# Kernel tuning notes

Measured on AMD Instinct MI355X. Metric: run time of the kernel, lower is better.

The kernel has to match this reference:

```python
import jax, jax.numpy as jnp
import numpy as np

H = 1024          # hidden_size
A = 8             # num_actions
T = 64            # timesteps
N = 256           # batch (num envs)


def _gru_cell(x, h, Wih, Whh, bih, bhh):
    # torch.nn.GRUCell math; gate order (r, z, n)
    gi = x @ Wih.T + bih           # [N, 3H]
    gh = h @ Whh.T + bhh           # [N, 3H]
    i_r, i_z, i_n = jnp.split(gi, 3, axis=1)
    h_r, h_z, h_n = jnp.split(gh, 3, axis=1)
    r = jax.nn.sigmoid(i_r + h_r)
    z = jax.nn.sigmoid(i_z + h_z)
    n = jnp.tanh(i_n + r * h_n)
    return (1.0 - z) * n + z * h


def setup_inputs() -> dict:
    key = jax.random.key(0)
    ks = jax.random.split(key, 12)
    s = 0.02
    return {
        "c": jax.random.normal(ks[0], (T * N, H), jnp.float32),
        "hxs": jax.random.normal(ks[1], (N, 3 * H), jnp.float32),
        "masks": jnp.ones((T * N, 1), jnp.float32),
        "prev_action_one_hot": jnp.zeros((T * N, A), jnp.float32).at[jnp.arange(T * N), jax.random.randint(ks[2], (T * N,), 0, A)].set(1.0),
        "h_gru_Wih": s * jax.random.normal(ks[3], (3 * H, H), jnp.float32),
        "h_gru_Whh": s * jax.random.normal(ks[4], (3 * H, H), jnp.float32),
        "h_gru_bih": jnp.zeros((3 * H,), jnp.float32),
        "h_gru_bhh": jnp.zeros((3 * H,), jnp.float32),
        "f_gru_Wih": s * jax.random.normal(ks[5], (3 * H, H), jnp.float32),
        "f_gru_Whh": s * jax.random.normal(ks[6], (3 * H, H), jnp.float32),
        "f_gru_bih": jnp.zeros((3 * H,), jnp.float32),
        "f_gru_bhh": jnp.zeros((3 * H,), jnp.float32),
        "p_W": s * jax.random.normal(ks[7], (2 * H, 2 * H + A), jnp.float32),
        "p_b": jnp.zeros((2 * H,), jnp.float32),
        "q_W": s * jax.random.normal(ks[8], (2 * H, 2 * H + A), jnp.float32),
        "q_b": jnp.zeros((2 * H,), jnp.float32),
    }


def reference(c, hxs, masks, prev_action_one_hot,
              h_gru_Wih, h_gru_Whh, h_gru_bih, h_gru_bhh,
              f_gru_Wih, f_gru_Whh, f_gru_bih, f_gru_bhh,
              p_W, p_b, q_W, q_b):
    c3 = c.reshape(T, N, H)
    m3 = masks.reshape(T, N, 1)
    a3 = prev_action_one_hot.reshape(T, N, A)
    f0 = hxs[:, :H]
    h0 = hxs[:, H:2 * H]
    q0 = hxs[:, 2 * H:]

    def step(carry, xs):
        f, h, q_mu = carry
        c_t, m_t, a_t = xs
        p_in = jnp.concatenate([h, q_mu, a_t], axis=1) * m_t
        p_dist = p_in @ p_W.T + p_b                     # [N, 2H]
        p_mu = p_dist[:, :H]
        q_in = jnp.concatenate([f, c_t, a_t], axis=1) * m_t
        q_dist = q_in @ q_W.T + q_b                     # [N, 2H]
        q_mu_new = q_dist[:, :H]
        f_new = _gru_cell(c_t, f * m_t, f_gru_Wih, f_gru_Whh, f_gru_bih, f_gru_bhh)
        h_new = _gru_cell(p_mu, h * m_t, h_gru_Wih, h_gru_Whh, h_gru_bih, h_gru_bhh)
        return (f_new, h_new, q_mu_new), (p_dist, q_dist)

    (f, h, q_mu), (p_all, q_all) = jax.lax.scan(step, (f0, h0, q0), (c3, m3, a3))
    acc_p = p_all.reshape(T * N, 2 * H)
    acc_q = q_all.reshape(T * N, 2 * H)
    hxs_out = jnp.concatenate([f, h, q_mu], axis=1)
    return acc_p, acc_q, hxs_out
```

## Files before the change

### kernel.cpp

```cpp
#include <hip/hip_runtime.h>
#include <math.h>

typedef __attribute__((ext_vector_type(8))) __bf16 bf16x8;
typedef __attribute__((ext_vector_type(4))) float f32x4;

constexpr int H = 1024, T = 64, NB = 256, TWOH = 2048, THREEH = 3072;
constexpr long long OFF_Q  = 33554432LL;
constexpr long long OFF_HX = 67108864LL;
constexpr int LA = 6;

constexpr int R_PWH = 0, R_PWQ = 2048, R_QWF = 4096, R_QWC = 6144,
              R_FWIH = 8192, R_FWHH = 11264, R_HWIH = 14336, R_HWHH = 17408;

#define LD4(p) (*reinterpret_cast<const float4*>(p))

__device__ __forceinline__ float sigf(float x) { return 1.0f / (1.0f + expf(-x)); }

__device__ __forceinline__ void gload16(const void* g, void* l) {
    __builtin_amdgcn_global_load_lds(
        (const __attribute__((address_space(1))) uint32_t*)g,
        (__attribute__((address_space(3))) uint32_t*)l, 16, 0, 0);
}

__device__ __forceinline__ void st_bf_swz(__bf16* base, int n, int k, float v) {
    base[(size_t)n * 1024 + (((k >> 3) ^ (n & 7)) << 3) + (k & 7)] = (__bf16)v;
}

#define FRAGOFF(rloc, gl) (((rloc) << 7) + ((((gl)) ^ ((rloc) & 7)) << 4))

template<int RT>
__device__ __forceinline__ void stage_tile(const char* g, char* l, int kb, int tid) {
    #pragma unroll
    for (int i = 0; i < RT / 32; ++i) {
        const int L = i * 4096 + tid * 16;
        gload16(g + (size_t)(L >> 7) * 2048 + (size_t)kb * 128 + (L & 127), l + L);
    }
}

__device__ __forceinline__ void mm128(
    int tid, char* sA, char* sB,
    const char* A0, const char* B0, int n0,
    const char* A1, const char* B1, int n1,
    f32x4 (&acc)[2][4])
{
    const int lane = tid & 63, w = tid >> 6;
    const int l15 = lane & 15, lg = lane >> 4;
    const int wr = w >> 1, wc = w & 1;
    const int nit = n0 + n1;
    int aoff[2][2], boff[4][2];
    #pragma unroll
    for (int fr = 0; fr < 2; ++fr)
        #pragma unroll
        for (int kk = 0; kk < 2; ++kk)
            aoff[fr][kk] = FRAGOFF(wr * 32 + fr * 16 + l15, kk * 4 + lg);
    #pragma unroll
    for (int fc = 0; fc < 4; ++fc)
        #pragma unroll
        for (int kk = 0; kk < 2; ++kk)
            boff[fc][kk] = FRAGOFF(wc * 64 + fc * 16 + l15, kk * 4 + lg);

    stage_tile<64>(A0, sA, 0, tid);
    stage_tile<128>(B0, sB, 0, tid);
    for (int kb = 0; kb < nit; ++kb) {
        const int kn = kb + 1;
        if (kn < nit) {
            const char* An = (kn < n0) ? A0 : A1;
            const char* Bn = (kn < n0) ? B0 : B1;
            const int kl = (kn < n0) ? kn : kn - n0;
            stage_tile<64>(An, sA + (kn & 1) * 8192, kl, tid);
            stage_tile<128>(Bn, sB + (kn & 1) * 16384, kl, tid);
            asm volatile("s_waitcnt vmcnt(6)" ::: "memory");
        } else {
            asm volatile("s_waitcnt vmcnt(0)" ::: "memory");
        }
        __builtin_amdgcn_s_barrier();
        __builtin_amdgcn_sched_barrier(0);
        char* Ab = sA + (kb & 1) * 8192;
        char* Bb = sB + (kb & 1) * 16384;
        bf16x8 af[2][2], bv[4][2];
        #pragma unroll
        for (int fr = 0; fr < 2; ++fr)
            #pragma unroll
            for (int kk = 0; kk < 2; ++kk)
                af[fr][kk] = *reinterpret_cast<const bf16x8*>(Ab + aoff[fr][kk]);
        #pragma unroll
        for (int fc = 0; fc < 4; ++fc)
            #pragma unroll
            for (int kk = 0; kk < 2; ++kk)
                bv[fc][kk] = *reinterpret_cast<const bf16x8*>(Bb + boff[fc][kk]);
        __builtin_amdgcn_s_setprio(1);
        #pragma unroll
        for (int kk = 0; kk < 2; ++kk)
            #pragma unroll
            for (int fr = 0; fr < 2; ++fr)
                #pragma unroll
                for (int fc = 0; fc < 4; ++fc)
                    acc[fr][fc] = __builtin_amdgcn_mfma_f32_16x16x32_bf16(
                        af[fr][kk], bv[fc][kk], acc[fr][fc], 0, 0, 0);
        __builtin_amdgcn_s_setprio(0);
        __builtin_amdgcn_s_barrier();
        __builtin_amdgcn_sched_barrier(0);
    }
}

__device__ __forceinline__ void mm32g1(
    int tid, char* sA, char* sB,
    const char* A, const char* Bg,
    f32x4 (&aR)[2], f32x4 (&aZ)[2], f32x4 (&aN)[2])
{
    const int lane = tid & 63, w = tid >> 6;
    const int l15 = lane & 15, lg = lane >> 4;
    const int wr = w >> 1, wc = w & 1;
    int aoff[2], boff[2][2];
    #pragma unroll
    for (int kk = 0; kk < 2; ++kk)
        aoff[kk] = FRAGOFF(wr * 16 + l15, kk * 4 + lg);
    #pragma unroll
    for (int fc = 0; fc < 2; ++fc)
        #pragma unroll
        for (int kk = 0; kk < 2; ++kk)
            boff[fc][kk] = FRAGOFF(wc * 32 + fc * 16 + l15, kk * 4 + lg);

    auto stg = [&](int buf, int kb) {
        stage_tile<32>(A, sA + buf * 4096, kb, tid);
        #pragma unroll
        for (int g = 0; g < 3; ++g)
            stage_tile<64>(Bg + (size_t)g * 2097152, sB + buf * 24576 + g * 8192, kb, tid);
    };
    stg(0, 0);
    for (int kb = 0; kb < 16; ++kb) {
        if (kb + 1 < 16) {
            stg((kb + 1) & 1, kb + 1);
            asm volatile("s_waitcnt vmcnt(7)" ::: "memory");
        } else {
            asm volatile("s_waitcnt vmcnt(0)" ::: "memory");
        }
        __builtin_amdgcn_s_barrier();
        __builtin_amdgcn_sched_barrier(0);
        char* Ab = sA + (kb & 1) * 4096;
        char* Bb = sB + (kb & 1) * 24576;
        bf16x8 af[2];
        #pragma unroll
        for (int kk = 0; kk < 2; ++kk)
            af[kk] = *reinterpret_cast<const bf16x8*>(Ab + aoff[kk]);
        bf16x8 bvr[2][2], bvz[2][2], bvn[2][2];
        #pragma unroll
        for (int fc = 0; fc < 2; ++fc)
            #pragma unroll
            for (int kk = 0; kk < 2; ++kk) {
                bvr[fc][kk] = *reinterpret_cast<const bf16x8*>(Bb + boff[fc][kk]);
                bvz[fc][kk] = *reinterpret_cast<const bf16x8*>(Bb + 8192 + boff[fc][kk]);
                bvn[fc][kk] = *reinterpret_cast<const bf16x8*>(Bb + 16384 + boff[fc][kk]);
            }
        __builtin_amdgcn_s_setprio(1);
        #pragma unroll
        for (int kk = 0; kk < 2; ++kk)
            #pragma unroll
            for (int fc = 0; fc < 2; ++fc) {
                aR[fc] = __builtin_amdgcn_mfma_f32_16x16x32_bf16(af[kk], bvr[fc][kk], aR[fc], 0, 0, 0);
                aZ[fc] = __builtin_amdgcn_mfma_f32_16x16x32_bf16(af[kk], bvz[fc][kk], aZ[fc], 0, 0, 0);
                aN[fc] = __builtin_amdgcn_mfma_f32_16x16x32_bf16(af[kk], bvn[fc][kk], aN[fc], 0, 0, 0);
            }
        __builtin_amdgcn_s_setprio(0);
        __builtin_amdgcn_s_barrier();
        __builtin_amdgcn_sched_barrier(0);
    }
}

__device__ __forceinline__ void do_xq(int slice, int i, int tid, char* sA, char* sB,
    const char* cbfB, const char* Wb, const float* act, const float* qW, float* out)
{
    const int lane = tid & 63, w = tid >> 6;
    const int l15 = lane & 15, lg = lane >> 4;
    const int wr = w >> 1, wc = w & 1;
    const int row0 = (i >> 4) * 64, col0 = (i & 15) * 128;
    const size_t grow0 = (size_t)slice * NB + row0;
    f32x4 acc[2][4] = {};
    mm128(tid, sA, sB, cbfB + grow0 * 2048, Wb + (size_t)(R_QWC + col0) * 2048, 16,
          nullptr, nullptr, 0, acc);
    #pragma unroll
    for (int fc = 0; fc < 4; ++fc) {
        const int gc = col0 + wc * 64 + fc * 16 + l15;
        const float* wp = qW + (size_t)gc * 2056 + 2048;
        float4 x0 = LD4(wp), x1 = LD4(wp + 4);
        #pragma unroll
        for (int fr = 0; fr < 2; ++fr)
            #pragma unroll
            for (int j = 0; j < 4; ++j) {
                const size_t n = grow0 + wr * 32 + fr * 16 + lg * 4 + j;
                const float* ar = act + n * 8;
                float4 a0 = LD4(ar), a1 = LD4(ar + 4);
                float dot = a0.x * x0.x + a0.y * x0.y + a0.z * x0.z + a0.w * x0.w
                          + a1.x * x1.x + a1.y * x1.y + a1.z * x1.z + a1.w * x1.w;
                out[OFF_Q + n * TWOH + gc] = acc[fr][fc][j] + dot;
            }
    }
}

__device__ __forceinline__ void do_gf(int slice, int i, int tid, char* sA, char* sB,
    const char* cbfB, const char* Wb, __bf16* Gfb)
{
    const int lane = tid & 63, w = tid >> 6;
    const int l15 = lane & 15, lg = lane >> 4;
    const int wr = w >> 1, wc = w & 1;
    const int row0 = (i / 24) * 64, col0 = (i % 24) * 128;
    f32x4 acc[2][4] = {};
    mm128(tid, sA, sB, cbfB + ((size_t)slice * NB + row0) * 2048,
          Wb + (size_t)(R_FWIH + col0) * 2048, 16, nullptr, nullptr, 0, acc);
    __bf16* gdst = Gfb + (size_t)(slice & 7) * NB * THREEH;
    #pragma unroll
    for (int fc = 0; fc < 4; ++fc) {
        const int gc = col0 + wc * 64 + fc * 16 + l15;
        #pragma unroll
        for (int fr = 0; fr < 2; ++fr)
            #pragma unroll
            for (int j = 0; j < 4; ++j) {
                const int n = row0 + wr * 32 + fr * 16 + lg * 4 + j;
                gdst[(size_t)n * THREEH + gc] = (__bf16)acc[fr][fc][j];
            }
    }
}

__global__ __launch_bounds__(256) void wcvt_k(
    const float* __restrict__ pW, const float* __restrict__ qW,
    const float* __restrict__ fWih, const float* __restrict__ fWhh,
    const float* __restrict__ hWih, const float* __restrict__ hWhh,
    __bf16* __restrict__ Wbf)
{
    const long i = (long)blockIdx.x * 256 + threadIdx.x;
    const int row = (int)(i >> 7);
    const int G   = (int)i & 127;
    const float* src; int stride; int koff = 0; int r;
    if (row < 2048)       { src = pW;   stride = 2056; koff = 0;    r = row; }
    else if (row < 4096)  { src = pW;   stride = 2056; koff = 1024; r = row - 2048; }
    else if (row < 6144)  { src = qW;   stride = 2056; koff = 0;    r = row - 4096; }
    else if (row < 8192)  { src = qW;   stride = 2056; koff = 1024; r = row - 6144; }
    else if (row < 11264) { src = fWih; stride = 1024; r = row - 8192; }
    else if (row < 14336) { src = fWhh; stride = 1024; r = row - 11264; }
    else if (row < 17408) { src = hWih; stride = 1024; r = row - 14336; }
    else                  { src = hWhh; stride = 1024; r = row - 17408; }
    const float* p = src + (long)r * stride + koff + G * 8;
    float4 a = LD4(p), b = LD4(p + 4);
    bf16x8 v;
    v[0] = (__bf16)a.x; v[1] = (__bf16)a.y; v[2] = (__bf16)a.z; v[3] = (__bf16)a.w;
    v[4] = (__bf16)b.x; v[5] = (__bf16)b.y; v[6] = (__bf16)b.z; v[7] = (__bf16)b.w;
    *reinterpret_cast<bf16x8*>(Wbf + (size_t)row * 1024 + ((G ^ (row & 7)) << 3)) = v;
}

__global__ __launch_bounds__(256) void ccvt_k(const float* __restrict__ c,
                                              __bf16* __restrict__ cbf) {
    const long i = (long)blockIdx.x * 256 + threadIdx.x;
    const int row = (int)(i >> 7);
    const int G   = (int)i & 127;
    const float* p = c + (size_t)row * 1024 + G * 8;
    float4 a = LD4(p), b = LD4(p + 4);
    bf16x8 v;
    v[0] = (__bf16)a.x; v[1] = (__bf16)a.y; v[2] = (__bf16)a.z; v[3] = (__bf16)a.w;
    v[4] = (__bf16)b.x; v[5] = (__bf16)b.y; v[6] = (__bf16)b.z; v[7] = (__bf16)b.w;
    *reinterpret_cast<bf16x8*>(cbf + (size_t)row * 1024 + ((G ^ (row & 7)) << 3)) = v;
}

__global__ __launch_bounds__(256) void init2_k(
    const float* __restrict__ hxs, const float* __restrict__ masks,
    float* __restrict__ fst0, float* __restrict__ hst0,
    __bf16* __restrict__ fbm0, __bf16* __restrict__ hbm0, __bf16* __restrict__ qmub0)
{
    const int idx = blockIdx.x * 256 + threadIdx.x;
    const int arr = idx >> 15;
    const int g   = idx & 32767;
    const int n   = g >> 7;
    const int G   = g & 127;
    const float m0 = masks[n];
    const float* p = hxs + (size_t)n * THREEH + arr * 1024 + G * 8;
    float4 a = LD4(p), b = LD4(p + 4);
    __bf16* dstB = arr == 0 ? fbm0 : (arr == 1 ? hbm0 : qmub0);
    bf16x8 v;
    v[0] = (__bf16)(a.x * m0); v[1] = (__bf16)(a.y * m0);
    v[2] = (__bf16)(a.z * m0); v[3] = (__bf16)(a.w * m0);
    v[4] = (__bf16)(b.x * m0); v[5] = (__bf16)(b.y * m0);
    v[6] = (__bf16)(b.z * m0); v[7] = (__bf16)(b.w * m0);
    *reinterpret_cast<bf16x8*>(dstB + (size_t)n * 1024 + ((G ^ (n & 7)) << 3)) = v;
    if (arr < 2) {
        float* dstF = arr == 0 ? fst0 : hst0;
        *reinterpret_cast<float4*>(dstF + (size_t)n * 1024 + G * 8) = a;
        *reinterpret_cast<float4*>(dstF + (size_t)n * 1024 + G * 8 + 4) = b;
    }
}

__global__ __launch_bounds__(256) void pre_k(
    const char* __restrict__ cbfB, const char* __restrict__ Wb,
    const float* __restrict__ act, const float* __restrict__ qW,
    __bf16* __restrict__ Gfb, float* __restrict__ out)
{
    __shared__ char smem[49152];
    const int s = blockIdx.x / 160;
    const int i = blockIdx.x % 160;
    if (i < 64) do_xq(s, i, threadIdx.x, smem, smem + 16384, cbfB, Wb, act, qW, out);
    else        do_gf(s, i - 64, threadIdx.x, smem, smem + 16384, cbfB, Wb, Gfb);
}

__global__ __launch_bounds__(256) void k1_k(
    int t, int hasFiller,
    const __bf16* __restrict__ hbm, const __bf16* __restrict__ qmub,
    __bf16* __restrict__ qmubN,
    const __bf16* __restrict__ fbm, const char* __restrict__ cbfB,
    const float* __restrict__ masks, const float* __restrict__ act,
    const float* __restrict__ pW, const float* __restrict__ pb,
    const float* __restrict__ qb, const float* __restrict__ qW,
    const char* __restrict__ Wb,
    __bf16* __restrict__ pmub, float* __restrict__ Shh, __bf16* __restrict__ Gfb,
    float* __restrict__ out)
{
    __shared__ char smem[49152];
    char* sA = smem;
    char* sB = smem + 16384;
    const int tid = threadIdx.x;
    const int lane = tid & 63, w = tid >> 6;
    const int l15 = lane & 15, lg = lane >> 4;
    const int wr = w >> 1, wc = w & 1;
    const float* mrow = masks + (size_t)t * NB;
    const float* mn   = masks + (size_t)(t + 1 < T ? t + 1 : t) * NB;
    int b = blockIdx.x;

    if (b < 64) {
        const int row0 = (b >> 4) * 64, col0 = (b & 15) * 128;
        f32x4 acc[2][4] = {};
        mm128(tid, sA, sB,
              (const char*)hbm + (size_t)row0 * 2048, Wb + (size_t)(R_PWH + col0) * 2048, 16,
              (const char*)qmub + (size_t)row0 * 2048, Wb + (size_t)(R_PWQ + col0) * 2048, 16,
              acc);
        float* ob = out + (size_t)t * NB * TWOH;
        #pragma unroll
        for (int fc = 0; fc < 4; ++fc) {
            const int gc = col0 + wc * 64 + fc * 16 + l15;
            const float* wp = pW + (size_t)gc * 2056 + 2048;
            float4 x0 = LD4(wp), x1 = LD4(wp + 4);
            const float bb = pb[gc];
            #pragma unroll
            for (int fr = 0; fr < 2; ++fr)
                #pragma unroll
                for (int j = 0; j < 4; ++j) {
                    const int n = row0 + wr * 32 + fr * 16 + lg * 4 + j;
                    const float* ar = act + ((size_t)t * NB + n) * 8;
                    float4 a0 = LD4(ar), a1 = LD4(ar + 4);
                    float dot = a0.x * x0.x + a0.y * x0.y + a0.z * x0.z + a0.w * x0.w
                              + a1.x * x1.x + a1.y * x1.y + a1.z * x1.z + a1.w * x1.w;
                    float v = acc[fr][fc][j] + mrow[n] * dot + bb;
                    ob[(size_t)n * TWOH + gc] = v;
                    if (gc < 1024) st_bf_swz(pmub, n, gc, v);
                }
        }
    } else if (b < 128) {
        b -= 64;
        const int row0 = (b >> 4) * 64, col0 = (b & 15) * 128;
        f32x4 acc[2][4] = {};
        mm128(tid, sA, sB,
              (const char*)fbm + (size_t)row0 * 2048, Wb + (size_t)(R_QWF + col0) * 2048, 16,
              nullptr, nullptr, 0, acc);
        float* ob = out + OFF_Q + (size_t)t * NB * TWOH;
        #pragma unroll
        for (int fc = 0; fc < 4; ++fc) {
            const int gc = col0 + wc * 64 + fc * 16 + l15;
            const float bb = qb[gc];
            #pragma unroll
            for (int fr = 0; fr < 2; ++fr)
                #pragma unroll
                for (int j = 0; j < 4; ++j) {
                    const int n = row0 + wr * 32 + fr * 16 + lg * 4 + j;
                    const float xq = ob[(size_t)n * TWOH + gc];
                    float v = acc[fr][fc][j] + mrow[n] * xq + bb;
                    ob[(size_t)n * TWOH + gc] = v;
                    if (gc < 1024) st_bf_swz(qmubN, n, gc, v * mn[n]);
                }
        }
    } else if (b < 224) {
        const int i = b - 128;
        const int row0 = (i / 24) * 64, col0 = (i % 24) * 128;
        f32x4 acc[2][4] = {};
        mm128(tid, sA, sB,
              (const char*)hbm + (size_t)row0 * 2048, Wb + (size_t)(R_HWHH + col0) * 2048, 16,
              nullptr, nullptr, 0, acc);
        #pragma unroll
        for (int fc = 0; fc < 4; ++fc) {
            const int gc = col0 + wc * 64 + fc * 16 + l15;
            #pragma unroll
            for (int fr = 0; fr < 2; ++fr)
                #pragma unroll
                for (int j = 0; j < 4; ++j) {
                    const int n = row0 + wr * 32 + fr * 16 + lg * 4 + j;
                    Shh[(size_t)n * THREEH + gc] = acc[fr][fc][j];
                }
        }
    } else if (b < 288) {
        if (hasFiller) do_xq(t + LA, b - 224, tid, sA, sB, cbfB, Wb, act, qW, out);
    } else {
        if (hasFiller) do_gf(t + LA, b - 288, tid, sA, sB, cbfB, Wb, Gfb);
    }
}

__global__ __launch_bounds__(256) void k2_k(
    int t,
    const __bf16* __restrict__ pmub, const __bf16* __restrict__ hbm,
    const __bf16* __restrict__ fbm,
    const float* __restrict__ Shh, const __bf16* __restrict__ Gfb,
    const float* __restrict__ hstF, float* __restrict__ hstN, __bf16* __restrict__ hbmN,
    const float* __restrict__ fstF, float* __restrict__ fstN, __bf16* __restrict__ fbmN,
    const char* __restrict__ Wb,
    const float* __restrict__ hbih, const float* __restrict__ hbhh,
    const float* __restrict__ fbih, const float* __restrict__ fbhh,
    const float* __restrict__ masks)
{
    __shared__ char smem[57344];
    char* sA = smem;
    char* sB = smem + 8192;
    const int tid = threadIdx.x;
    const int lane = tid & 63, w = tid >> 6;
    const int l15 = lane & 15, lg = lane >> 4;
    const int wr = w >> 1, wc = w & 1;
    const float* mrow = masks + (size_t)t * NB;
    const float* mn   = masks + (size_t)(t + 1 < T ? t + 1 : t) * NB;
    const int b = blockIdx.x;
    const int i = b & 127;
    const int row0 = (i >> 4) * 32, col0 = (i & 15) * 64;

    f32x4 aR[2] = {}, aZ[2] = {}, aN[2] = {};
    if (b < 128) {
        mm32g1(tid, sA, sB,
               (const char*)pmub + (size_t)row0 * 2048,
               Wb + (size_t)(R_HWIH + col0) * 2048, aR, aZ, aN);
        #pragma unroll
        for (int fc = 0; fc < 2; ++fc) {
            const int col = col0 + wc * 32 + fc * 16 + l15;
            const float bri = hbih[col],        brh = hbhh[col];
            const float bzi = hbih[col + 1024], bzh = hbhh[col + 1024];
            const float bni = hbih[col + 2048], bnh = hbhh[col + 2048];
            #pragma unroll
            for (int j = 0; j < 4; ++j) {
                const int n = row0 + wr * 16 + lg * 4 + j;
                const float ghr = Shh[(size_t)n * THREEH + col];
                const float ghz = Shh[(size_t)n * THREEH + col + 1024];
                const float ghn = Shh[(size_t)n * THREEH + col + 2048];
                const float rg = sigf(aR[fc][j] + bri + ghr + brh);
                const float zg = sigf(aZ[fc][j] + bzi + ghz + bzh);
                const float ng = tanhf(aN[fc][j] + bni + rg * (ghn + bnh));
                const float hm = hstF[(size_t)n * 1024 + col] * mrow[n];
                const float o = (1.f - zg) * ng + zg * hm;
                hstN[(size_t)n * 1024 + col] = o;
                st_bf_swz(hbmN, n, col, o * mn[n]);
            }
        }
    } else {
        mm32g1(tid, sA, sB,
               (const char*)fbm + (size_t)row0 * 2048,
               Wb + (size_t)(R_FWHH + col0) * 2048, aR, aZ, aN);
        const __bf16* gsl = Gfb + (size_t)(t & 7) * NB * THREEH;
        #pragma unroll
        for (int fc = 0; fc < 2; ++fc) {
            const int col = col0 + wc * 32 + fc * 16 + l15;
            const float br  = fbih[col] + fbhh[col];
            const float bz  = fbih[col + 1024] + fbhh[col + 1024];
            const float bni = fbih[col + 2048], bnh = fbhh[col + 2048];
            #pragma unroll
            for (int j = 0; j < 4; ++j) {
                const int n = row0 + wr * 16 + lg * 4 + j;
                const float gfr = (float)gsl[(size_t)n * THREEH + col];
                const float gfz = (float)gsl[(size_t)n * THREEH + col + 1024];
                const float gfn = (float)gsl[(size_t)n * THREEH + col + 2048];
                const float rg = sigf(gfr + aR[fc][j] + br);
                const float zg = sigf(gfz + aZ[fc][j] + bz);
                const float ng = tanhf(gfn + bni + rg * (aN[fc][j] + bnh));
                const float fm = fstF[(size_t)n * 1024 + col] * mrow[n];
                const float o = (1.f - zg) * ng + zg * fm;
                fstN[(size_t)n * 1024 + col] = o;
                st_bf_swz(fbmN, n, col, o * mn[n]);
            }
        }
    }
}

__global__ __launch_bounds__(256) void write_hxs_k(const float* __restrict__ fS,
                                                   const float* __restrict__ hS,
                                                   float* out) {
    const int i = blockIdx.x * 256 + threadIdx.x;
    const int n = i / THREEH;
    const int j = i - n * THREEH;
    float v;
    if (j < H)          v = fS[(size_t)n * H + j];
    else if (j < TWOH)  v = hS[(size_t)n * H + (j - H)];
    else                v = out[OFF_Q + ((size_t)(T - 1) * NB + n) * TWOH + (j - TWOH)];
    out[OFF_HX + i] = v;
}

extern "C" void kernel_launch(void* const* d_in, const int* in_sizes, int n_in,
                              void* d_out, int out_size, void* d_ws, size_t ws_size,
                              hipStream_t stream) {
    (void)in_sizes; (void)n_in; (void)out_size; (void)ws_size;

    const float* c     = (const float*)d_in[0];
    const float* hxs   = (const float*)d_in[1];
    const float* masks = (const float*)d_in[2];
    const float* act   = (const float*)d_in[3];
    const float* hWih  = (const float*)d_in[4];
    const float* hWhh  = (const float*)d_in[5];
    const float* hbih  = (const float*)d_in[6];
    const float* hbhh  = (const float*)d_in[7];
    const float* fWih  = (const float*)d_in[8];
    const float* fWhh  = (const float*)d_in[9];
    const float* fbih  = (const float*)d_in[10];
    const float* fbhh  = (const float*)d_in[11];
    const float* pW    = (const float*)d_in[12];
    const float* pb    = (const float*)d_in[13];
    const float* qW    = (const float*)d_in[14];
    const float* qb    = (const float*)d_in[15];

    float* out = (float*)d_out;
    char*  wsb = (char*)d_ws;

    __bf16* Wbf  = (__bf16*)(wsb);
    __bf16* cbf  = (__bf16*)(wsb + 41943040LL);
    float*  fst[2] = { (float*)(wsb + 75497472LL), (float*)(wsb + 76546048LL) };
    float*  hst[2] = { (float*)(wsb + 77594624LL), (float*)(wsb + 78643200LL) };
    __bf16* fbm[2] = { (__bf16*)(wsb + 79691776LL), (__bf16*)(wsb + 80216064LL) };
    __bf16* hbm[2] = { (__bf16*)(wsb + 80740352LL), (__bf16*)(wsb + 81264640LL) };
    __bf16* qmb[2] = { (__bf16*)(wsb + 81788928LL), (__bf16*)(wsb + 82313216LL) };
    __bf16* pmub   = (__bf16*)(wsb + 82837504LL);
    float*  Shh    = (float*)(wsb + 83361792LL);
    __bf16* Gfb    = (__bf16*)(wsb + 86507520LL);
    const char* Wb = (const char*)Wbf;
    const char* cbfB = (const char*)cbf;

    wcvt_k <<<dim3(10240), dim3(256), 0, stream>>>(pW, qW, fWih, fWhh, hWih, hWhh, Wbf);
    ccvt_k <<<dim3(8192),  dim3(256), 0, stream>>>(c, cbf);
    init2_k<<<dim3(384),   dim3(256), 0, stream>>>(hxs, masks, fst[0], hst[0],
                                                   fbm[0], hbm[0], qmb[0]);
    pre_k  <<<dim3(LA * 160), dim3(256), 0, stream>>>(cbfB, Wb, act, qW, Gfb, out);

    for (int t = 0; t < T; ++t) {
        const int cur = t & 1, nxt = cur ^ 1;
        const int hasF = (t + LA < T) ? 1 : 0;
        k1_k<<<dim3(hasF ? 384 : 224), dim3(256), 0, stream>>>(
            t, hasF, hbm[cur], qmb[cur], qmb[nxt], fbm[cur], cbfB,
            masks, act, pW, pb, qb, qW, Wb, pmub, Shh, Gfb, out);
        k2_k<<<dim3(256), dim3(256), 0, stream>>>(
            t, pmub, hbm[cur], fbm[cur], Shh, Gfb,
            hst[cur], hst[nxt], hbm[nxt],
            fst[cur], fst[nxt], fbm[nxt],
            Wb, hbih, hbhh, fbih, fbhh, masks);
    }

    write_hxs_k<<<dim3(3072), dim3(256), 0, stream>>>(fst[0], hst[0], out);
}
```

Before: 2.271 ms.

## Rebalance recurrent schedule across kernels and triple-buffer GEMM LDS staging

Moves the f-GRU recurrent cell from the second per-step kernel into the first, and moves the q_mu half of the p projection (plus action and bias terms) into the second kernel for step t+1, alongside the lookahead xq/gf filler work. The first kernel now only adds the h-part GEMM to the partial p result already in the output. Both kernels launch 352 blocks, so the critical path per step is shorter and the per-step work is more even. The shared GEMM helper now uses a three-stage LDS ring with prefetch distance two, at the cost of more shared memory per block (72KB), which can lower occupancy.

```diff
diff --git a/kernel.cpp b/kernel.cpp
--- a/kernel.cpp
+++ b/kernel.cpp
@@ -39,14 +39,12 @@
 
 __device__ __forceinline__ void mm128(
     int tid, char* sA, char* sB,
-    const char* A0, const char* B0, int n0,
-    const char* A1, const char* B1, int n1,
+    const char* A, const char* B, int nit,
     f32x4 (&acc)[2][4])
 {
     const int lane = tid & 63, w = tid >> 6;
     const int l15 = lane & 15, lg = lane >> 4;
     const int wr = w >> 1, wc = w & 1;
-    const int nit = n0 + n1;
     int aoff[2][2], boff[4][2];
     #pragma unroll
     for (int fr = 0; fr < 2; ++fr)
@@ -59,24 +57,29 @@
         for (int kk = 0; kk < 2; ++kk)
             boff[fc][kk] = FRAGOFF(wc * 64 + fc * 16 + l15, kk * 4 + lg);
 
-    stage_tile<64>(A0, sA, 0, tid);
-    stage_tile<128>(B0, sB, 0, tid);
+    stage_tile<64>(A, sA, 0, tid);
+    stage_tile<128>(B, sB, 0, tid);
+    if (nit > 1) {
+        stage_tile<64>(A, sA + 8192, 1, tid);
+        stage_tile<128>(B, sB + 16384, 1, tid);
+    }
     for (int kb = 0; kb < nit; ++kb) {
-        const int kn = kb + 1;
+        const int kn = kb + 2;
         if (kn < nit) {
-            const char* An = (kn < n0) ? A0 : A1;
-            const char* Bn = (kn < n0) ? B0 : B1;
-            const int kl = (kn < n0) ? kn : kn - n0;
-            stage_tile<64>(An, sA + (kn & 1) * 8192, kl, tid);
-            stage_tile<128>(Bn, sB + (kn & 1) * 16384, kl, tid);
+            const int bo = kn % 3;
+            stage_tile<64>(A, sA + bo * 8192, kn, tid);
+            stage_tile<128>(B, sB + bo * 16384, kn, tid);
+            asm volatile("s_waitcnt vmcnt(12)" ::: "memory");
+        } else if (kb + 1 < nit) {
             asm volatile("s_waitcnt vmcnt(6)" ::: "memory");
         } else {
             asm volatile("s_waitcnt vmcnt(0)" ::: "memory");
         }
         __builtin_amdgcn_s_barrier();
         __builtin_amdgcn_sched_barrier(0);
-        char* Ab = sA + (kb & 1) * 8192;
-        char* Bb = sB + (kb & 1) * 16384;
+        const int bc = kb % 3;
+        char* Ab = sA + bc * 8192;
+        char* Bb = sB + bc * 16384;
         bf16x8 af[2][2], bv[4][2];
         #pragma unroll
         for (int fr = 0; fr < 2; ++fr)
@@ -176,8 +179,7 @@
     const int row0 = (i >> 4) * 64, col0 = (i & 15) * 128;
     const size_t grow0 = (size_t)slice * NB + row0;
     f32x4 acc[2][4] = {};
-    mm128(tid, sA, sB, cbfB + grow0 * 2048, Wb + (size_t)(R_QWC + col0) * 2048, 16,
-          nullptr, nullptr, 0, acc);
+    mm128(tid, sA, sB, cbfB + grow0 * 2048, Wb + (size_t)(R_QWC + col0) * 2048, 16, acc);
     #pragma unroll
     for (int fc = 0; fc < 4; ++fc) {
         const int gc = col0 + wc * 64 + fc * 16 + l15;
@@ -206,7 +208,7 @@
     const int row0 = (i / 24) * 64, col0 = (i % 24) * 128;
     f32x4 acc[2][4] = {};
     mm128(tid, sA, sB, cbfB + ((size_t)slice * NB + row0) * 2048,
-          Wb + (size_t)(R_FWIH + col0) * 2048, 16, nullptr, nullptr, 0, acc);
+          Wb + (size_t)(R_FWIH + col0) * 2048, 16, acc);
     __bf16* gdst = Gfb + (size_t)(slice & 7) * NB * THREEH;
     #pragma unroll
     for (int fc = 0; fc < 4; ++fc) {
@@ -217,6 +219,39 @@
             for (int j = 0; j < 4; ++j) {
                 const int n = row0 + wr * 32 + fr * 16 + lg * 4 + j;
                 gdst[(size_t)n * THREEH + gc] = (__bf16)acc[fr][fc][j];
+            }
+    }
+}
+
+__device__ __forceinline__ void do_pq(int tt, int i, int tid, char* sA, char* sB,
+    const __bf16* qmu_t, const char* Wb, const float* masks, const float* act,
+    const float* pW, const float* pb, float* out)
+{
+    const int lane = tid & 63, w = tid >> 6;
+    const int l15 = lane & 15, lg = lane >> 4;
+    const int wr = w >> 1, wc = w & 1;
+    const int row0 = (i >> 4) * 64, col0 = (i & 15) * 128;
+    f32x4 acc[2][4] = {};
+    mm128(tid, sA, sB, (const char*)qmu_t + (size_t)row0 * 2048,
+          Wb + (size_t)(R_PWQ + col0) * 2048, 16, acc);
+    const float* mrow = masks + (size_t)tt * NB;
+    float* ob = out + (size_t)tt * NB * TWOH;
+    #pragma unroll
+    for (int fc = 0; fc < 4; ++fc) {
+        const int gc = col0 + wc * 64 + fc * 16 + l15;
+        const float* wp = pW + (size_t)gc * 2056 + 2048;
+        float4 x0 = LD4(wp), x1 = LD4(wp + 4);
+        const float bb = pb[gc];
+        #pragma unroll
+        for (int fr = 0; fr < 2; ++fr)
+            #pragma unroll
+            for (int j = 0; j < 4; ++j) {
+                const int n = row0 + wr * 32 + fr * 16 + lg * 4 + j;
+                const float* ar = act + ((size_t)tt * NB + n) * 8;
+                float4 a0 = LD4(ar), a1 = LD4(ar + 4);
+                float dot = a0.x * x0.x + a0.y * x0.y + a0.z * x0.z + a0.w * x0.w
+                          + a1.x * x1.x + a1.y * x1.y + a1.z * x1.z + a1.w * x1.w;
+                ob[(size_t)n * TWOH + gc] = acc[fr][fc][j] + mrow[n] * dot + bb;
             }
     }
 }
@@ -290,30 +325,38 @@
 __global__ __launch_bounds__(256) void pre_k(
     const char* __restrict__ cbfB, const char* __restrict__ Wb,
     const float* __restrict__ act, const float* __restrict__ qW,
+    const __bf16* __restrict__ qmb0, const float* __restrict__ masks,
+    const float* __restrict__ pW, const float* __restrict__ pb,
     __bf16* __restrict__ Gfb, float* __restrict__ out)
 {
-    __shared__ char smem[49152];
-    const int s = blockIdx.x / 160;
-    const int i = blockIdx.x % 160;
-    if (i < 64) do_xq(s, i, threadIdx.x, smem, smem + 16384, cbfB, Wb, act, qW, out);
-    else        do_gf(s, i - 64, threadIdx.x, smem, smem + 16384, cbfB, Wb, Gfb);
+    __shared__ char smem[73728];
+    if (blockIdx.x < LA * 160) {
+        const int s = blockIdx.x / 160;
+        const int i = blockIdx.x % 160;
+        if (i < 64) do_xq(s, i, threadIdx.x, smem, smem + 24576, cbfB, Wb, act, qW, out);
+        else        do_gf(s, i - 64, threadIdx.x, smem, smem + 24576, cbfB, Wb, Gfb);
+    } else {
+        do_pq(0, blockIdx.x - LA * 160, threadIdx.x, smem, smem + 24576,
+              qmb0, Wb, masks, act, pW, pb, out);
+    }
 }
 
 __global__ __launch_bounds__(256) void k1_k(
-    int t, int hasFiller,
-    const __bf16* __restrict__ hbm, const __bf16* __restrict__ qmub,
+    int t,
+    const __bf16* __restrict__ hbm, const __bf16* __restrict__ fbm,
     __bf16* __restrict__ qmubN,
-    const __bf16* __restrict__ fbm, const char* __restrict__ cbfB,
     const float* __restrict__ masks, const float* __restrict__ act,
-    const float* __restrict__ pW, const float* __restrict__ pb,
     const float* __restrict__ qb, const float* __restrict__ qW,
     const char* __restrict__ Wb,
-    __bf16* __restrict__ pmub, float* __restrict__ Shh, __bf16* __restrict__ Gfb,
+    __bf16* __restrict__ pmub, float* __restrict__ Shh,
+    const __bf16* __restrict__ Gfb,
+    const float* __restrict__ fbih, const float* __restrict__ fbhh,
+    const float* __restrict__ fstF, float* __restrict__ fstN, __bf16* __restrict__ fbmN,
     float* __restrict__ out)
 {
-    __shared__ char smem[49152];
+    __shared__ char smem[73728];
     char* sA = smem;
-    char* sB = smem + 16384;
+    char* sB = smem + 24576;
     const int tid = threadIdx.x;
     const int lane = tid & 63, w = tid >> 6;
     const int l15 = lane & 15, lg = lane >> 4;
@@ -326,26 +369,18 @@
         const int row0 = (b >> 4) * 64, col0 = (b & 15) * 128;
         f32x4 acc[2][4] = {};
         mm128(tid, sA, sB,
-              (const char*)hbm + (size_t)row0 * 2048, Wb + (size_t)(R_PWH + col0) * 2048, 16,
-              (const char*)qmub + (size_t)row0 * 2048, Wb + (size_t)(R_PWQ + col0) * 2048, 16,
-              acc);
+              (const char*)hbm + (size_t)row0 * 2048,
+              Wb + (size_t)(R_PWH + col0) * 2048, 16, acc);
         float* ob = out + (size_t)t * NB * TWOH;
         #pragma unroll
         for (int fc = 0; fc < 4; ++fc) {
             const int gc = col0 + wc * 64 + fc * 16 + l15;
-            const float* wp = pW + (size_t)gc * 2056 + 2048;
-            float4 x0 = LD4(wp), x1 = LD4(wp + 4);
-            const float bb = pb[gc];
             #pragma unroll
             for (int fr = 0; fr < 2; ++fr)
                 #pragma unroll
                 for (int j = 0; j < 4; ++j) {
                     const int n = row0 + wr * 32 + fr * 16 + lg * 4 + j;
-                    const float* ar = act + ((size_t)t * NB + n) * 8;
-                    float4 a0 = LD4(ar), a1 = LD4(ar + 4);
-                    float dot = a0.x * x0.x + a0.y * x0.y + a0.z * x0.z + a0.w * x0.w
-                              + a1.x * x1.x + a1.y * x1.y + a1.z * x1.z + a1.w * x1.w;
-                    float v = acc[fr][fc][j] + mrow[n] * dot + bb;
+                    const float v = ob[(size_t)n * TWOH + gc] + acc[fr][fc][j];
                     ob[(size_t)n * TWOH + gc] = v;
                     if (gc < 1024) st_bf_swz(pmub, n, gc, v);
                 }
@@ -355,8 +390,8 @@
         const int row0 = (b >> 4) * 64, col0 = (b & 15) * 128;
         f32x4 acc[2][4] = {};
         mm128(tid, sA, sB,
-              (const char*)fbm + (size_t)row0 * 2048, Wb + (size_t)(R_QWF + col0) * 2048, 16,
-              nullptr, nullptr, 0, acc);
+              (const char*)fbm + (size_t)row0 * 2048,
+              Wb + (size_t)(R_QWF + col0) * 2048, 16, acc);
         float* ob = out + OFF_Q + (size_t)t * NB * TWOH;
         #pragma unroll
         for (int fc = 0; fc < 4; ++fc) {
@@ -378,8 +413,8 @@
         const int row0 = (i / 24) * 64, col0 = (i % 24) * 128;
         f32x4 acc[2][4] = {};
         mm128(tid, sA, sB,
-              (const char*)hbm + (size_t)row0 * 2048, Wb + (size_t)(R_HWHH + col0) * 2048, 16,
-              nullptr, nullptr, 0, acc);
+              (const char*)hbm + (size_t)row0 * 2048,
+              Wb + (size_t)(R_HWHH + col0) * 2048, 16, acc);
         #pragma unroll
         for (int fc = 0; fc < 4; ++fc) {
             const int gc = col0 + wc * 64 + fc * 16 + l15;
@@ -391,28 +426,54 @@
                     Shh[(size_t)n * THREEH + gc] = acc[fr][fc][j];
                 }
         }
-    } else if (b < 288) {
-        if (hasFiller) do_xq(t + LA, b - 224, tid, sA, sB, cbfB, Wb, act, qW, out);
     } else {
-        if (hasFiller) do_gf(t + LA, b - 288, tid, sA, sB, cbfB, Wb, Gfb);
+        const int i = b - 224;
+        const int row0 = (i >> 4) * 32, col0 = (i & 15) * 64;
+        f32x4 aR[2] = {}, aZ[2] = {}, aN[2] = {};
+        mm32g1(tid, sA, sB,
+               (const char*)fbm + (size_t)row0 * 2048,
+               Wb + (size_t)(R_FWHH + col0) * 2048, aR, aZ, aN);
+        const __bf16* gsl = Gfb + (size_t)(t & 7) * NB * THREEH;
+        #pragma unroll
+        for (int fc = 0; fc < 2; ++fc) {
+            const int col = col0 + wc * 32 + fc * 16 + l15;
+            const float br  = fbih[col] + fbhh[col];
+            const float bz  = fbih[col + 1024] + fbhh[col + 1024];
+            const float bni = fbih[col + 2048], bnh = fbhh[col + 2048];
+            #pragma unroll
+            for (int j = 0; j < 4; ++j) {
+                const int n = row0 + wr * 16 + lg * 4 + j;
+                const float gfr = (float)gsl[(size_t)n * THREEH + col];
+                const float gfz = (float)gsl[(size_t)n * THREEH + col + 1024];
+                const float gfn = (float)gsl[(size_t)n * THREEH + col + 2048];
+                const float rg = sigf(gfr + aR[fc][j] + br);
+                const float zg = sigf(gfz + aZ[fc][j] + bz);
+                const float ng = tanhf(gfn + bni + rg * (aN[fc][j] + bnh));
+                const float fm = fstF[(size_t)n * 1024 + col] * mrow[n];
+                const float o = (1.f - zg) * ng + zg * fm;
+                fstN[(size_t)n * 1024 + col] = o;
+                st_bf_swz(fbmN, n, col, o * mn[n]);
+            }
+        }
     }
 }
 
 __global__ __launch_bounds__(256) void k2_k(
     int t,
-    const __bf16* __restrict__ pmub, const __bf16* __restrict__ hbm,
-    const __bf16* __restrict__ fbm,
-    const float* __restrict__ Shh, const __bf16* __restrict__ Gfb,
+    const __bf16* __restrict__ pmub, const __bf16* __restrict__ qmubN,
+    const char* __restrict__ cbfB,
+    const float* __restrict__ Shh,
     const float* __restrict__ hstF, float* __restrict__ hstN, __bf16* __restrict__ hbmN,
-    const float* __restrict__ fstF, float* __restrict__ fstN, __bf16* __restrict__ fbmN,
     const char* __restrict__ Wb,
     const float* __restrict__ hbih, const float* __restrict__ hbhh,
-    const float* __restrict__ fbih, const float* __restrict__ fbhh,
-    const float* __restrict__ masks)
-{
-    __shared__ char smem[57344];
+    const float* __restrict__ masks, const float* __restrict__ act,
+    const float* __restrict__ pW, const float* __restrict__ pb,
+    const float* __restrict__ qW,
+    __bf16* __restrict__ Gfb, float* __restrict__ out)
+{
+    __shared__ char smem[73728];
     char* sA = smem;
-    char* sB = smem + 8192;
+    char* sB = smem + 24576;
     const int tid = threadIdx.x;
     const int lane = tid & 63, w = tid >> 6;
     const int l15 = lane & 15, lg = lane >> 4;
@@ -420,11 +481,10 @@
     const float* mrow = masks + (size_t)t * NB;
     const float* mn   = masks + (size_t)(t + 1 < T ? t + 1 : t) * NB;
     const int b = blockIdx.x;
-    const int i = b & 127;
-    const int row0 = (i >> 4) * 32, col0 = (i & 15) * 64;
-
-    f32x4 aR[2] = {}, aZ[2] = {}, aN[2] = {};
+
     if (b < 128) {
+        const int row0 = (b >> 4) * 32, col0 = (b & 15) * 64;
+        f32x4 aR[2] = {}, aZ[2] = {}, aN[2] = {};
         mm32g1(tid, sA, sB,
                (const char*)pmub + (size_t)row0 * 2048,
                Wb + (size_t)(R_HWIH + col0) * 2048, aR, aZ, aN);
@@ -449,32 +509,15 @@
                 st_bf_swz(hbmN, n, col, o * mn[n]);
             }
         }
+    } else if (b < 192) {
+        if (t + 1 < T)
+            do_pq(t + 1, b - 128, tid, sA, sB, qmubN, Wb, masks, act, pW, pb, out);
+    } else if (b < 256) {
+        if (t + LA < T)
+            do_xq(t + LA, b - 192, tid, sA, sB, cbfB, Wb, act, qW, out);
     } else {
-        mm32g1(tid, sA, sB,
-               (const char*)fbm + (size_t)row0 * 2048,
-               Wb + (size_t)(R_FWHH + col0) * 2048, aR, aZ, aN);
-        const __bf16* gsl = Gfb + (size_t)(t & 7) * NB * THREEH;
-        #pragma unroll
-        for (int fc = 0; fc < 2; ++fc) {
-            const int col = col0 + wc * 32 + fc * 16 + l15;
-            const float br  = fbih[col] + fbhh[col];
-            const float bz  = fbih[col + 1024] + fbhh[col + 1024];
-            const float bni = fbih[col + 2048], bnh = fbhh[col + 2048];
-            #pragma unroll
-            for (int j = 0; j < 4; ++j) {
-                const int n = row0 + wr * 16 + lg * 4 + j;
-                const float gfr = (float)gsl[(size_t)n * THREEH + col];
-                const float gfz = (float)gsl[(size_t)n * THREEH + col + 1024];
-                const float gfn = (float)gsl[(size_t)n * THREEH + col + 2048];
-                const float rg = sigf(gfr + aR[fc][j] + br);
-                const float zg = sigf(gfz + aZ[fc][j] + bz);
-                const float ng = tanhf(gfn + bni + rg * (aN[fc][j] + bnh));
-                const float fm = fstF[(size_t)n * 1024 + col] * mrow[n];
-                const float o = (1.f - zg) * ng + zg * fm;
-                fstN[(size_t)n * 1024 + col] = o;
-                st_bf_swz(fbmN, n, col, o * mn[n]);
-            }
-        }
+        if (t + LA < T)
+            do_gf(t + LA, b - 256, tid, sA, sB, cbfB, Wb, Gfb);
     }
 }
 
@@ -526,26 +569,26 @@
     __bf16* pmub   = (__bf16*)(wsb + 82837504LL);
     float*  Shh    = (float*)(wsb + 83361792LL);
     __bf16* Gfb    = (__bf16*)(wsb + 86507520LL);
-    const char* Wb = (const char*)Wbf;
+    const char* Wb   = (const char*)Wbf;
     const char* cbfB = (const char*)cbf;
 
     wcvt_k <<<dim3(10240), dim3(256), 0, stream>>>(pW, qW, fWih, fWhh, hWih, hWhh, Wbf);
     ccvt_k <<<dim3(8192),  dim3(256), 0, stream>>>(c, cbf);
     init2_k<<<dim3(384),   dim3(256), 0, stream>>>(hxs, masks, fst[0], hst[0],
                                                    fbm[0], hbm[0], qmb[0]);
-    pre_k  <<<dim3(LA * 160), dim3(256), 0, stream>>>(cbfB, Wb, act, qW, Gfb, out);
+    pre_k  <<<dim3(LA * 160 + 64), dim3(256), 0, stream>>>(
+        cbfB, Wb, act, qW, qmb[0], masks, pW, pb, Gfb, out);
 
     for (int t = 0; t < T; ++t) {
         const int cur = t & 1, nxt = cur ^ 1;
-        const int hasF = (t + LA < T) ? 1 : 0;
-        k1_k<<<dim3(hasF ? 384 : 224), dim3(256), 0, stream>>>(
-            t, hasF, hbm[cur], qmb[cur], qmb[nxt], fbm[cur], cbfB,
-            masks, act, pW, pb, qb, qW, Wb, pmub, Shh, Gfb, out);
-        k2_k<<<dim3(256), dim3(256), 0, stream>>>(
-            t, pmub, hbm[cur], fbm[cur], Shh, Gfb,
+        k1_k<<<dim3(352), dim3(256), 0, stream>>>(
+            t, hbm[cur], fbm[cur], qmb[nxt],
+            masks, act, qb, qW, Wb, pmub, Shh, Gfb,
+            fbih, fbhh, fst[cur], fst[nxt], fbm[nxt], out);
+        k2_k<<<dim3(352), dim3(256), 0, stream>>>(
+            t, pmub, qmb[nxt], cbfB, Shh,
             hst[cur], hst[nxt], hbm[nxt],
-            fst[cur], fst[nxt], fbm[nxt],
-            Wb, hbih, hbhh, fbih, fbhh, masks);
+            Wb, hbih, hbhh, masks, act, pW, pb, qW, Gfb, out);
     }
 
     write_hxs_k<<<dim3(3072), dim3(256), 0, stream>>>(fst[0], hst[0], out);
```

New measurement: 2.107 ms. -7.2%, faster.
